# Optimization experiments

Hardware: AMD Instinct MI355X
Metric: run time of the kernel (lower is better)

Reference implementation:

```python
import jax, jax.numpy as jnp
import numpy as np


def _filt2d(img, k):
    # 2D cross-correlation with OpenCV's default BORDER_REFLECT_101 padding.
    # img: [H, W], k: [3, 3]. XLA conv is cross-correlation (no flip), matching cv2.
    p = jnp.pad(img, 1, mode='reflect')  # reflect == REFLECT_101
    return jax.lax.conv_general_dilated(p[None, None], k[None, None],
                                        window_strides=(1, 1), padding='VALID')[0, 0]


def setup_inputs() -> dict:
    key = jax.random.key(0)
    k1, k2 = jax.random.split(key)
    pred = jax.random.normal(k1, (1, 1, 4096, 4096), dtype=jnp.float32)
    target = jax.random.normal(k2, (1, 1, 4096, 4096), dtype=jnp.float32)
    return {"pred": pred, "target": target}


def reference(pred, target):
    alpha = 0.2  # forward default
    # ---- masked MSE over target > 0 (named MAE in the original) ----
    valid = target > 0
    diff = jnp.where(valid, target - pred, 0.0)
    n_valid = jnp.maximum(jnp.sum(valid), 1)
    mae = jnp.sum(diff * diff) / n_valid.astype(diff.dtype)
    # ---- edge term: GaussianBlur(3x3, sigma=0) then Sobel x/y (cv2 semantics) ----
    g1 = jnp.array([0.25, 0.5, 0.25], jnp.float32)  # cv2 fixed 3-tap Gaussian
    blur_k = jnp.outer(g1, g1)
    smooth = jnp.array([1.0, 2.0, 1.0], jnp.float32)
    deriv = jnp.array([-1.0, 0.0, 1.0], jnp.float32)
    sob_x = jnp.outer(smooth, deriv)   # d/dx: smooth rows, differentiate cols
    sob_y = jnp.outer(deriv, smooth)   # d/dy
    p2 = jnp.squeeze(pred)   # [H, W]
    t2 = jnp.squeeze(target)
    pb = _filt2d(p2, blur_k)
    tb = _filt2d(t2, blur_k)
    dx = _filt2d(pb, sob_x) - _filt2d(tb, sob_x)
    dy = _filt2d(pb, sob_y) - _filt2d(tb, sob_y)
    # NOTE: original subtracts the y term (as written in the source) — kept faithfully.
    G = jnp.mean(dx * dx - dy * dy)
    # In torch the edge term goes through a numpy round-trip (no gradient).
    G = jax.lax.stop_gradient(G)
    return alpha * G + (1.0 - alpha) * mae
```

## Files before the change

### kernel.cpp

```cpp
#include <hip/hip_runtime.h>


#define TW 256
#define TH 8
#define LROWS 12
#define LW 264

__device__ __forceinline__ int reflect101(int i, int n) {
    if (i < 0) i = -i;
    if (i >= n) i = 2 * n - 2 - i;
    return i;
}

__device__ __forceinline__ void async16(const float* g, float* l) {
    __builtin_amdgcn_global_load_lds(
        (const __attribute__((address_space(1))) void*)g,
        (__attribute__((address_space(3))) void*)l,
        16, 0, 0);
}

__global__ __launch_bounds__(256, 4) void loss_main(
    const float* __restrict__ pred, const float* __restrict__ target,
    float* __restrict__ part, int H, int W)
{
    __shared__ float psh[LROWS][LW];
    __shared__ float tsh[LROWS][LW];
    __shared__ float partials[4][3];

    const int tid  = threadIdx.x;
    const int lane = tid & 63;
    const int w    = tid >> 6;
    const int r0 = blockIdx.y * TH;
    const int c0 = blockIdx.x * TW;

#pragma unroll
    for (int j = 0; j < 6; ++j) {
        const int idx = j * 4 + w;
        const int row = (idx >= 12) ? idx - 12 : idx;
        const int gr  = reflect101(r0 - 2 + row, H);
        const size_t goff = (size_t)gr * W + c0 + lane * 4;
        if (idx >= 12) async16(target + goff, &tsh[row][4]);
        else           async16(pred   + goff, &psh[row][4]);
    }

    if (tid < 48) {
        const int row = tid >> 2;
        const int hc  = tid & 3;
        const int lc  = (hc < 2) ? (2 + hc) : (258 + hc);
        const int gc  = reflect101((hc < 2) ? (c0 - 2 + hc)
                                            : (c0 + 254 + hc), W);
        const int gr  = reflect101(r0 - 2 + row, H);
        const size_t off = (size_t)gr * W + gc;
        psh[row][lc] = pred[off];
        tsh[row][lc] = target[off];
    }
    __syncthreads();

    const int cg = lane;
    const int rb = w * 2;
    float mse = 0.f, cnt = 0.f, g = 0.f;

    float4 D0, D1, D2, D3, D4, S0, S1, S2, S3, S4;

    auto hpass = [&](int rw, bool doMse, float4& D_, float4& S_) {
        const float4 p0 = *(const float4*)&psh[rw][4 * cg];
        const float4 p1 = *(const float4*)&psh[rw][4 * cg + 4];
        const float4 p2 = *(const float4*)&psh[rw][4 * cg + 8];
        const float4 t0 = *(const float4*)&tsh[rw][4 * cg];
        const float4 t1 = *(const float4*)&tsh[rw][4 * cg + 4];
        const float4 t2 = *(const float4*)&tsh[rw][4 * cg + 8];
        const float e0z = p0.z - t0.z, e0w = p0.w - t0.w;
        const float e1x = p1.x - t1.x, e1y = p1.y - t1.y;
        const float e1z = p1.z - t1.z, e1w = p1.w - t1.w;
        const float e2x = p2.x - t2.x, e2y = p2.y - t2.y;
        D_.x = 0.25f * (e1z - e0z) + 0.5f * (e1y - e0w);
        D_.y = 0.25f * (e1w - e0w) + 0.5f * (e1z - e1x);
        D_.z = 0.25f * (e2x - e1x) + 0.5f * (e1w - e1y);
        D_.w = 0.25f * (e2y - e1y) + 0.5f * (e2x - e1z);
        S_.x = 0.25f * (e0z + e1z) + (e0w + e1y) + 1.5f * e1x;
        S_.y = 0.25f * (e0w + e1w) + (e1x + e1z) + 1.5f * e1y;
        S_.z = 0.25f * (e1x + e2x) + (e1y + e1w) + 1.5f * e1z;
        S_.w = 0.25f * (e1y + e2y) + (e1z + e2x) + 1.5f * e1w;
        if (doMse) {
            if (t1.x > 0.f) { mse += e1x * e1x; cnt += 1.f; }
            if (t1.y > 0.f) { mse += e1y * e1y; cnt += 1.f; }
            if (t1.z > 0.f) { mse += e1z * e1z; cnt += 1.f; }
            if (t1.w > 0.f) { mse += e1w * e1w; cnt += 1.f; }
        }
    };

    hpass(rb + 0, false, D0, S0);
    hpass(rb + 1, false, D1, S1);
    hpass(rb + 2, true,  D2, S2);
    hpass(rb + 3, true,  D3, S3);

#pragma unroll
    for (int k = 0; k < 2; ++k) {
        hpass(rb + 4 + k, false, D4, S4);
        const float dx0 = 0.25f * (D0.x + D4.x) + (D1.x + D3.x) + 1.5f * D2.x;
        const float dx1 = 0.25f * (D0.y + D4.y) + (D1.y + D3.y) + 1.5f * D2.y;
        const float dx2 = 0.25f * (D0.z + D4.z) + (D1.z + D3.z) + 1.5f * D2.z;
        const float dx3 = 0.25f * (D0.w + D4.w) + (D1.w + D3.w) + 1.5f * D2.w;
        const float dy0 = 0.25f * (S4.x - S0.x) + 0.5f * (S3.x - S1.x);
        const float dy1 = 0.25f * (S4.y - S0.y) + 0.5f * (S3.y - S1.y);
        const float dy2 = 0.25f * (S4.z - S0.z) + 0.5f * (S3.z - S1.z);
        const float dy3 = 0.25f * (S4.w - S0.w) + 0.5f * (S3.w - S1.w);
        g += (dx0 * dx0 - dy0 * dy0) + (dx1 * dx1 - dy1 * dy1)
           + (dx2 * dx2 - dy2 * dy2) + (dx3 * dx3 - dy3 * dy3);
        D0 = D1; D1 = D2; D2 = D3; D3 = D4;
        S0 = S1; S1 = S2; S2 = S3; S3 = S4;
    }

    for (int off = 32; off > 0; off >>= 1) {
        mse += __shfl_down(mse, off, 64);
        cnt += __shfl_down(cnt, off, 64);
        g   += __shfl_down(g,   off, 64);
    }
    if (lane == 0) {
        partials[w][0] = mse;
        partials[w][1] = cnt;
        partials[w][2] = g;
    }
    __syncthreads();
    if (tid == 0) {
        float m = 0.f, c2 = 0.f, gg = 0.f;
        for (int wv = 0; wv < 4; ++wv) {
            m  += partials[wv][0];
            c2 += partials[wv][1];
            gg += partials[wv][2];
        }
        const int bid = blockIdx.y * gridDim.x + blockIdx.x;
        float* slot = part + 3 * bid;
        slot[0] = m;
        slot[1] = c2;
        slot[2] = gg;
    }
}

__global__ __launch_bounds__(256) void loss_final(
    const float* __restrict__ part, int nslots,
    float* __restrict__ out, double inv_hw)
{
    __shared__ double red[4][3];
    double m = 0.0, c = 0.0, g = 0.0;
    for (int s = threadIdx.x; s < nslots; s += 256) {
        m += (double)part[3 * s];
        c += (double)part[3 * s + 1];
        g += (double)part[3 * s + 2];
    }
    for (int off = 32; off > 0; off >>= 1) {
        m += __shfl_down(m, off, 64);
        c += __shfl_down(c, off, 64);
        g += __shfl_down(g, off, 64);
    }
    const int w = threadIdx.x >> 6;
    if ((threadIdx.x & 63) == 0) { red[w][0] = m; red[w][1] = c; red[w][2] = g; }
    __syncthreads();
    if (threadIdx.x == 0) {
        m = red[0][0] + red[1][0] + red[2][0] + red[3][0];
        c = red[0][1] + red[1][1] + red[2][1] + red[3][1];
        g = red[0][2] + red[1][2] + red[2][2] + red[3][2];
        const double cnt = c < 1.0 ? 1.0 : c;
        out[0] = (float)(0.2 * (g * inv_hw) + 0.8 * (m / cnt));
    }
}

extern "C" void kernel_launch(void* const* d_in, const int* in_sizes, int n_in,
                              void* d_out, int out_size, void* d_ws, size_t ws_size,
                              hipStream_t stream) {
    const float* pred   = (const float*)d_in[0];
    const float* target = (const float*)d_in[1];
    float* out  = (float*)d_out;
    float* part = (float*)d_ws;

    const int H = 4096, W = 4096;
    const int nblocks = (W / TW) * (H / TH);

    dim3 grid(W / TW, H / TH);
    loss_main<<<grid, 256, 0, stream>>>(pred, target, part, H, W);
    loss_final<<<1, 256, 0, stream>>>(part, nblocks, out,
                                      1.0 / ((double)H * (double)W));
}
```

Baseline: 151.7 us.

## Compute horizontal pass once per row and share via LDS for vertical pass

Each wave previously recomputed the horizontal filter pass for 6 rows, so halo rows were redundantly processed by overlapping waves (24 row-passes for 12 rows). Now each of the 12 rows is horizontally filtered exactly once, the results are written back into the shared tiles, and the vertical pass reads 5 rows from LDS. This removes redundant LDS reads and ALU work at the cost of two extra block barriers and extra LDS write/read traffic. The launch-bounds occupancy hint is also dropped.

```diff
diff --git a/kernel.cpp b/kernel.cpp
--- a/kernel.cpp
+++ b/kernel.cpp
@@ -19,7 +19,7 @@
         16, 0, 0);
 }
 
-__global__ __launch_bounds__(256, 4) void loss_main(
+__global__ __launch_bounds__(256) void loss_main(
     const float* __restrict__ pred, const float* __restrict__ target,
     float* __restrict__ part, int H, int W)
 {
@@ -56,59 +56,70 @@
     }
     __syncthreads();
 
-    const int cg = lane;
-    const int rb = w * 2;
     float mse = 0.f, cnt = 0.f, g = 0.f;
 
-    float4 D0, D1, D2, D3, D4, S0, S1, S2, S3, S4;
-
-    auto hpass = [&](int rw, bool doMse, float4& D_, float4& S_) {
-        const float4 p0 = *(const float4*)&psh[rw][4 * cg];
-        const float4 p1 = *(const float4*)&psh[rw][4 * cg + 4];
-        const float4 p2 = *(const float4*)&psh[rw][4 * cg + 8];
-        const float4 t0 = *(const float4*)&tsh[rw][4 * cg];
-        const float4 t1 = *(const float4*)&tsh[rw][4 * cg + 4];
-        const float4 t2 = *(const float4*)&tsh[rw][4 * cg + 8];
+    float4 Dh[3], Sh[3];
+#pragma unroll
+    for (int i = 0; i < 3; ++i) {
+        const int row = i * 4 + w;
+        const float4 p0 = *(const float4*)&psh[row][4 * lane];
+        const float4 p1 = *(const float4*)&psh[row][4 * lane + 4];
+        const float4 p2 = *(const float4*)&psh[row][4 * lane + 8];
+        const float4 t0 = *(const float4*)&tsh[row][4 * lane];
+        const float4 t1 = *(const float4*)&tsh[row][4 * lane + 4];
+        const float4 t2 = *(const float4*)&tsh[row][4 * lane + 8];
         const float e0z = p0.z - t0.z, e0w = p0.w - t0.w;
         const float e1x = p1.x - t1.x, e1y = p1.y - t1.y;
         const float e1z = p1.z - t1.z, e1w = p1.w - t1.w;
         const float e2x = p2.x - t2.x, e2y = p2.y - t2.y;
-        D_.x = 0.25f * (e1z - e0z) + 0.5f * (e1y - e0w);
-        D_.y = 0.25f * (e1w - e0w) + 0.5f * (e1z - e1x);
-        D_.z = 0.25f * (e2x - e1x) + 0.5f * (e1w - e1y);
-        D_.w = 0.25f * (e2y - e1y) + 0.5f * (e2x - e1z);
-        S_.x = 0.25f * (e0z + e1z) + (e0w + e1y) + 1.5f * e1x;
-        S_.y = 0.25f * (e0w + e1w) + (e1x + e1z) + 1.5f * e1y;
-        S_.z = 0.25f * (e1x + e2x) + (e1y + e1w) + 1.5f * e1z;
-        S_.w = 0.25f * (e1y + e2y) + (e1z + e2x) + 1.5f * e1w;
-        if (doMse) {
+        Dh[i].x = 0.25f * (e1z - e0z) + 0.5f * (e1y - e0w);
+        Dh[i].y = 0.25f * (e1w - e0w) + 0.5f * (e1z - e1x);
+        Dh[i].z = 0.25f * (e2x - e1x) + 0.5f * (e1w - e1y);
+        Dh[i].w = 0.25f * (e2y - e1y) + 0.5f * (e2x - e1z);
+        Sh[i].x = 0.25f * (e0z + e1z) + (e0w + e1y) + 1.5f * e1x;
+        Sh[i].y = 0.25f * (e0w + e1w) + (e1x + e1z) + 1.5f * e1y;
+        Sh[i].z = 0.25f * (e1x + e2x) + (e1y + e1w) + 1.5f * e1z;
+        Sh[i].w = 0.25f * (e1y + e2y) + (e1z + e2x) + 1.5f * e1w;
+        if (row >= 2 && row < 10) {
             if (t1.x > 0.f) { mse += e1x * e1x; cnt += 1.f; }
             if (t1.y > 0.f) { mse += e1y * e1y; cnt += 1.f; }
             if (t1.z > 0.f) { mse += e1z * e1z; cnt += 1.f; }
             if (t1.w > 0.f) { mse += e1w * e1w; cnt += 1.f; }
         }
-    };
-
-    hpass(rb + 0, false, D0, S0);
-    hpass(rb + 1, false, D1, S1);
-    hpass(rb + 2, true,  D2, S2);
-    hpass(rb + 3, true,  D3, S3);
+    }
+    __syncthreads();
 
 #pragma unroll
-    for (int k = 0; k < 2; ++k) {
-        hpass(rb + 4 + k, false, D4, S4);
-        const float dx0 = 0.25f * (D0.x + D4.x) + (D1.x + D3.x) + 1.5f * D2.x;
-        const float dx1 = 0.25f * (D0.y + D4.y) + (D1.y + D3.y) + 1.5f * D2.y;
-        const float dx2 = 0.25f * (D0.z + D4.z) + (D1.z + D3.z) + 1.5f * D2.z;
-        const float dx3 = 0.25f * (D0.w + D4.w) + (D1.w + D3.w) + 1.5f * D2.w;
-        const float dy0 = 0.25f * (S4.x - S0.x) + 0.5f * (S3.x - S1.x);
-        const float dy1 = 0.25f * (S4.y - S0.y) + 0.5f * (S3.y - S1.y);
-        const float dy2 = 0.25f * (S4.z - S0.z) + 0.5f * (S3.z - S1.z);
-        const float dy3 = 0.25f * (S4.w - S0.w) + 0.5f * (S3.w - S1.w);
+    for (int i = 0; i < 3; ++i) {
+        const int row = i * 4 + w;
+        *(float4*)&psh[row][4 + 4 * lane] = Dh[i];
+        *(float4*)&tsh[row][4 + 4 * lane] = Sh[i];
+    }
+    __syncthreads();
+
+#pragma unroll
+    for (int i = 0; i < 2; ++i) {
+        const int ro = 2 + i * 4 + w;
+        const float4 d0 = *(const float4*)&psh[ro - 2][4 + 4 * lane];
+        const float4 d1 = *(const float4*)&psh[ro - 1][4 + 4 * lane];
+        const float4 d2 = *(const float4*)&psh[ro    ][4 + 4 * lane];
+        const float4 d3 = *(const float4*)&psh[ro + 1][4 + 4 * lane];
+        const float4 d4 = *(const float4*)&psh[ro + 2][4 + 4 * lane];
+        const float4 s0 = *(const float4*)&tsh[ro - 2][4 + 4 * lane];
+        const float4 s1 = *(const float4*)&tsh[ro - 1][4 + 4 * lane];
+        const float4 s2 = *(const float4*)&tsh[ro    ][4 + 4 * lane];
+        const float4 s3 = *(const float4*)&tsh[ro + 1][4 + 4 * lane];
+        const float4 s4 = *(const float4*)&tsh[ro + 2][4 + 4 * lane];
+        const float dx0 = 0.25f * (d0.x + d4.x) + (d1.x + d3.x) + 1.5f * d2.x;
+        const float dx1 = 0.25f * (d0.y + d4.y) + (d1.y + d3.y) + 1.5f * d2.y;
+        const float dx2 = 0.25f * (d0.z + d4.z) + (d1.z + d3.z) + 1.5f * d2.z;
+        const float dx3 = 0.25f * (d0.w + d4.w) + (d1.w + d3.w) + 1.5f * d2.w;
+        const float dy0 = 0.25f * (s4.x - s0.x) + 0.5f * (s3.x - s1.x);
+        const float dy1 = 0.25f * (s4.y - s0.y) + 0.5f * (s3.y - s1.y);
+        const float dy2 = 0.25f * (s4.z - s0.z) + 0.5f * (s3.z - s1.z);
+        const float dy3 = 0.25f * (s4.w - s0.w) + 0.5f * (s3.w - s1.w);
         g += (dx0 * dx0 - dy0 * dy0) + (dx1 * dx1 - dy1 * dy1)
            + (dx2 * dx2 - dy2 * dy2) + (dx3 * dx3 - dy3 * dy3);
-        D0 = D1; D1 = D2; D2 = D3; D3 = D4;
-        S0 = S1; S1 = S2; S2 = S3; S3 = S4;
     }
 
     for (int off = 32; off > 0; off >>= 1) {
```

Result: no change. 150.3 us (-0.9%).

## Stage pred-target difference in LDS and double tile height

Applied to the files above, without the earlier changes.

Each tile now loads pred and target into registers, computes the difference e and the masked MSE directly from those registers, and stores only e into a single shared array. The async global-to-LDS copies are dropped. Tile height grows from 8 to 16 rows, so the halo overhead falls from 12 loaded rows per 8 output rows to 20 per 16. This halves LDS footprint and LDS reads and cuts redundant halo traffic. In exchange the loads are now synchronous register loads, each block does more serial work, and the min-blocks launch bound is removed.

```diff
diff --git a/kernel.cpp b/kernel.cpp
--- a/kernel.cpp
+++ b/kernel.cpp
@@ -2,8 +2,8 @@
 
 
 #define TW 256
-#define TH 8
-#define LROWS 12
+#define TH 16
+#define LROWS 20
 #define LW 264
 
 __device__ __forceinline__ int reflect101(int i, int n) {
@@ -12,19 +12,11 @@
     return i;
 }
 
-__device__ __forceinline__ void async16(const float* g, float* l) {
-    __builtin_amdgcn_global_load_lds(
-        (const __attribute__((address_space(1))) void*)g,
-        (__attribute__((address_space(3))) void*)l,
-        16, 0, 0);
-}
-
-__global__ __launch_bounds__(256, 4) void loss_main(
+__global__ __launch_bounds__(256) void loss_main(
     const float* __restrict__ pred, const float* __restrict__ target,
     float* __restrict__ part, int H, int W)
 {
-    __shared__ float psh[LROWS][LW];
-    __shared__ float tsh[LROWS][LW];
+    __shared__ float esh[LROWS][LW];
     __shared__ float partials[4][3];
 
     const int tid  = threadIdx.x;
@@ -33,17 +25,29 @@
     const int r0 = blockIdx.y * TH;
     const int c0 = blockIdx.x * TW;
 
+    float mse = 0.f, cnt = 0.f, g = 0.f;
+
 #pragma unroll
-    for (int j = 0; j < 6; ++j) {
-        const int idx = j * 4 + w;
-        const int row = (idx >= 12) ? idx - 12 : idx;
+    for (int i = 0; i < 5; ++i) {
+        const int idx = i * 256 + tid;
+        const int row = idx >> 6;
+        const int cg  = idx & 63;
         const int gr  = reflect101(r0 - 2 + row, H);
-        const size_t goff = (size_t)gr * W + c0 + lane * 4;
-        if (idx >= 12) async16(target + goff, &tsh[row][4]);
-        else           async16(pred   + goff, &psh[row][4]);
+        const size_t off = (size_t)gr * W + c0 + cg * 4;
+        const float4 p = *(const float4*)(pred + off);
+        const float4 t = *(const float4*)(target + off);
+        const float4 e = make_float4(p.x - t.x, p.y - t.y,
+                                     p.z - t.z, p.w - t.w);
+        if (row >= 2 && row < 18) {
+            if (t.x > 0.f) { mse += e.x * e.x; cnt += 1.f; }
+            if (t.y > 0.f) { mse += e.y * e.y; cnt += 1.f; }
+            if (t.z > 0.f) { mse += e.z * e.z; cnt += 1.f; }
+            if (t.w > 0.f) { mse += e.w * e.w; cnt += 1.f; }
+        }
+        *(float4*)&esh[row][4 + 4 * cg] = e;
     }
 
-    if (tid < 48) {
+    if (tid < 80) {
         const int row = tid >> 2;
         const int hc  = tid & 3;
         const int lc  = (hc < 2) ? (2 + hc) : (258 + hc);
@@ -51,52 +55,35 @@
                                             : (c0 + 254 + hc), W);
         const int gr  = reflect101(r0 - 2 + row, H);
         const size_t off = (size_t)gr * W + gc;
-        psh[row][lc] = pred[off];
-        tsh[row][lc] = target[off];
+        esh[row][lc] = pred[off] - target[off];
     }
     __syncthreads();
 
-    const int cg = lane;
-    const int rb = w * 2;
-    float mse = 0.f, cnt = 0.f, g = 0.f;
-
+    const int wb = 4 * w;
     float4 D0, D1, D2, D3, D4, S0, S1, S2, S3, S4;
 
-    auto hpass = [&](int rw, bool doMse, float4& D_, float4& S_) {
-        const float4 p0 = *(const float4*)&psh[rw][4 * cg];
-        const float4 p1 = *(const float4*)&psh[rw][4 * cg + 4];
-        const float4 p2 = *(const float4*)&psh[rw][4 * cg + 8];
-        const float4 t0 = *(const float4*)&tsh[rw][4 * cg];
-        const float4 t1 = *(const float4*)&tsh[rw][4 * cg + 4];
-        const float4 t2 = *(const float4*)&tsh[rw][4 * cg + 8];
-        const float e0z = p0.z - t0.z, e0w = p0.w - t0.w;
-        const float e1x = p1.x - t1.x, e1y = p1.y - t1.y;
-        const float e1z = p1.z - t1.z, e1w = p1.w - t1.w;
-        const float e2x = p2.x - t2.x, e2y = p2.y - t2.y;
-        D_.x = 0.25f * (e1z - e0z) + 0.5f * (e1y - e0w);
-        D_.y = 0.25f * (e1w - e0w) + 0.5f * (e1z - e1x);
-        D_.z = 0.25f * (e2x - e1x) + 0.5f * (e1w - e1y);
-        D_.w = 0.25f * (e2y - e1y) + 0.5f * (e2x - e1z);
-        S_.x = 0.25f * (e0z + e1z) + (e0w + e1y) + 1.5f * e1x;
-        S_.y = 0.25f * (e0w + e1w) + (e1x + e1z) + 1.5f * e1y;
-        S_.z = 0.25f * (e1x + e2x) + (e1y + e1w) + 1.5f * e1z;
-        S_.w = 0.25f * (e1y + e2y) + (e1z + e2x) + 1.5f * e1w;
-        if (doMse) {
-            if (t1.x > 0.f) { mse += e1x * e1x; cnt += 1.f; }
-            if (t1.y > 0.f) { mse += e1y * e1y; cnt += 1.f; }
-            if (t1.z > 0.f) { mse += e1z * e1z; cnt += 1.f; }
-            if (t1.w > 0.f) { mse += e1w * e1w; cnt += 1.f; }
-        }
+    auto hp = [&](int rw, float4& D_, float4& S_) {
+        const float4 f0 = *(const float4*)&esh[rw][4 * lane];
+        const float4 f1 = *(const float4*)&esh[rw][4 * lane + 4];
+        const float4 f2 = *(const float4*)&esh[rw][4 * lane + 8];
+        D_.x = 0.25f * (f1.z - f0.z) + 0.5f * (f1.y - f0.w);
+        D_.y = 0.25f * (f1.w - f0.w) + 0.5f * (f1.z - f1.x);
+        D_.z = 0.25f * (f2.x - f1.x) + 0.5f * (f1.w - f1.y);
+        D_.w = 0.25f * (f2.y - f1.y) + 0.5f * (f2.x - f1.z);
+        S_.x = 0.25f * (f0.z + f1.z) + (f0.w + f1.y) + 1.5f * f1.x;
+        S_.y = 0.25f * (f0.w + f1.w) + (f1.x + f1.z) + 1.5f * f1.y;
+        S_.z = 0.25f * (f1.x + f2.x) + (f1.y + f1.w) + 1.5f * f1.z;
+        S_.w = 0.25f * (f1.y + f2.y) + (f1.z + f2.x) + 1.5f * f1.w;
     };
 
-    hpass(rb + 0, false, D0, S0);
-    hpass(rb + 1, false, D1, S1);
-    hpass(rb + 2, true,  D2, S2);
-    hpass(rb + 3, true,  D3, S3);
+    hp(wb + 0, D0, S0);
+    hp(wb + 1, D1, S1);
+    hp(wb + 2, D2, S2);
+    hp(wb + 3, D3, S3);
 
 #pragma unroll
-    for (int k = 0; k < 2; ++k) {
-        hpass(rb + 4 + k, false, D4, S4);
+    for (int k = 0; k < 4; ++k) {
+        hp(wb + 4 + k, D4, S4);
         const float dx0 = 0.25f * (D0.x + D4.x) + (D1.x + D3.x) + 1.5f * D2.x;
         const float dx1 = 0.25f * (D0.y + D4.y) + (D1.y + D3.y) + 1.5f * D2.y;
         const float dx2 = 0.25f * (D0.z + D4.z) + (D1.z + D3.z) + 1.5f * D2.z;
@@ -174,9 +161,9 @@
     float* part = (float*)d_ws;
 
     const int H = 4096, W = 4096;
-    const int nblocks = (W / TW) * (H / TH);
 
     dim3 grid(W / TW, H / TH);
+    const int nblocks = grid.x * grid.y;
     loss_main<<<grid, 256, 0, stream>>>(pred, target, part, H, W);
     loss_final<<<1, 256, 0, stream>>>(part, nblocks, out,
                                       1.0 / ((double)H * (double)W));
```

New measurement: 154.7 us. Within noise of the previous version (+2.0%).
